# Kernel optimization log

Measured on AMD Instinct MI355X. Metric: run time of the kernel, lower is better.

Reference implementation:

```python
import jax, jax.numpy as jnp
import numpy as np
from jax import lax

NUM_SEGMENTS = 50
HIDDEN = 128
IN_CH = 64
LOGSIG_DIM = IN_CH + IN_CH * (IN_CH - 1) // 2 + IN_CH  # level1 + Levy area + startpoint


def setup_inputs() -> dict:
    key = jax.random.key(0)
    k0, k1, k2, k3, k4 = jax.random.split(key, 5)
    B, C, T, V = 16, IN_CH, 200, 25
    x = jax.random.normal(k0, (B, C, T, V), dtype=jnp.float32)
    s = 1.0 / np.sqrt(HIDDEN).astype(np.float32)
    W_ih = jax.random.uniform(k1, (4 * HIDDEN, LOGSIG_DIM), jnp.float32, -s, s)
    W_hh = jax.random.uniform(k2, (4 * HIDDEN, HIDDEN), jnp.float32, -s, s)
    b_ih = jax.random.uniform(k3, (4 * HIDDEN,), jnp.float32, -s, s)
    b_hh = jax.random.uniform(k4, (4 * HIDDEN,), jnp.float32, -s, s)
    return {"x": x, "W_ih": W_ih, "W_hh": W_hh, "b_ih": b_ih, "b_hh": b_hh}


def _segment_logsig(xn):
    # xn: (N, C, T). Split T into NUM_SEGMENTS chunks; level-2 log-signature per chunk.
    N, C, T = xn.shape
    L = T // NUM_SEGMENTS  # points per segment
    p = xn.transpose(0, 2, 1).reshape(N, NUM_SEGMENTS, L, C)  # path points
    start = p[:, :, 0]                                  # (N,S,C) segment startpoint
    inc = p[:, :, 1:] - p[:, :, :-1]                    # (N,S,L-1,C) increments
    dev = p[:, :, :-1] - start[:, :, None]              # (N,S,L-1,C) p_t - p_0
    # Level-2 iterated integrals (cross terms): S2_ij = sum_t dev_t,i * inc_t,j
    S2 = jnp.einsum('nsti,nstj->nsij', dev, inc)        # (N,S,C,C)
    A = 0.5 * (S2 - S2.transpose(0, 1, 3, 2))           # Levy area (antisymmetric part)
    iu, ju = jnp.triu_indices(C, k=1)
    levy = A[:, :, iu, ju]                              # (N,S,C(C-1)/2)
    lvl1 = p[:, :, -1] - start                          # (N,S,C) level-1 term
    return jnp.concatenate([lvl1, levy, start], axis=-1)  # (N,S,LOGSIG_DIM)


def _lstm(seq, W_ih, W_hh, b_ih, b_hh):
    # seq: (N, S, F). Single-layer unidirectional LSTM, torch gate order (i,f,g,o).
    N = seq.shape[0]
    x_proj = jnp.einsum('nsf,gf->nsg', seq, W_ih) + b_ih + b_hh  # (N,S,4H)

    def step(carry, xt):
        h, c = carry
        gates = xt + h @ W_hh.T
        i, f, g, o = jnp.split(gates, 4, axis=-1)
        c = jax.nn.sigmoid(f) * c + jax.nn.sigmoid(i) * jnp.tanh(g)
        h = jax.nn.sigmoid(o) * jnp.tanh(c)
        return (h, c), h

    h0 = jnp.zeros((N, HIDDEN), seq.dtype)
    c0 = jnp.zeros((N, HIDDEN), seq.dtype)
    _, hs = lax.scan(step, (h0, c0), x_proj.transpose(1, 0, 2))
    return hs.transpose(1, 0, 2)  # (N,S,H)


def reference(x, W_ih, W_hh, b_ih, b_hh):
    B, C, T, V = x.shape
    xn = x.transpose(0, 3, 1, 2).reshape(B * V, C, T)
    ls = _segment_logsig(xn)                      # (B*V, S, LOGSIG_DIM)
    h = _lstm(ls, W_ih, W_hh, b_ih, b_hh)          # (B*V, S, H)
    out = h.reshape(B, V, NUM_SEGMENTS, HIDDEN).transpose(0, 3, 2, 1)
    return out  # (B, H, S, V)
```

## Files before the change

kernel.cpp:

```cpp
#include <hip/hip_runtime.h>
#include <stdint.h>

#define NSEG 50
#define HID 128
#define KDIM 2144
#define KD2 2240
#define KD2B 4480
#define NROW 20000
#define NROW_PAD 20000
#define GATES 512
#define NSEQ 400
#define NGRP 528

typedef __attribute__((ext_vector_type(8))) _Float16 f16x8;
typedef __attribute__((ext_vector_type(4))) _Float16 f16x4;
typedef __attribute__((ext_vector_type(4))) float f32x4;
typedef __attribute__((ext_vector_type(4))) uint32_t u32x4;

#define GLB_SPACE __attribute__((address_space(1)))
#define LDS_SPACE __attribute__((address_space(3)))

__device__ __forceinline__ void g2lds16(const void* g, void* l) {
    __builtin_amdgcn_global_load_lds((const GLB_SPACE uint32_t*)g,
                                     (LDS_SPACE uint32_t*)l, 16, 0, 0);
}

__device__ __forceinline__ int goff528(int i) {
    int n = 63 - i;
    int q = n >> 2, t = n & 3;
    return NGRP - (q + 1) * (2 * q + t);
}
__device__ __forceinline__ int ifromg(int g) {
    int i = 63 - (int)sqrtf(8.0f * (float)(NGRP - g));
    if (i < 0) i = 0;
    if (i > 62) i = 62;
    while (i > 0 && goff528(i) > g) i--;
    while (goff528(i + 1) <= g) i++;
    return i;
}

#define UVP(c) ((((c) & 3) << 4) | ((c) >> 2))

__global__ __launch_bounds__(512) void feat_kernel(const float* __restrict__ x,
                                                   const float* __restrict__ Wih,
                                                   const float* __restrict__ Whh,
                                                   const float* __restrict__ bih,
                                                   const float* __restrict__ bhh,
                                                   _Float16* __restrict__ feat,
                                                   _Float16* __restrict__ wh,
                                                   _Float16* __restrict__ whh16,
                                                   float* __restrict__ bias) {
    int bid = blockIdx.x;
    int tid = threadIdx.x;

    __shared__ float pbuf[64 * 101];
    __shared__ __align__(16) float4 uv4[25 * 64];

    if (bid >= 800) {
        int* kmap = (int*)pbuf;
        for (int k = tid; k < KD2; k += 512) {
            int orig;
            if (k < 64) {
                orig = k;
            } else if (k < 64 + 4 * NGRP) {
                int g = (k - 64) >> 2, p = (k - 64) & 3;
                int i = ifromg(g);
                int j = i + 1 + 4 * (g - goff528(i)) + p;
                orig = (j < 64) ? (64 + 63 * i - (i * (i - 1)) / 2 + (j - i - 1)) : -1;
            } else {
                orig = 2080 + (k - (64 + 4 * NGRP));
            }
            kmap[k] = orig;
        }
        __syncthreads();
        const int nwih = 512 * KD2;
        const int nwhh = 512 * HID;
        const int total = nwih + nwhh + 512;
        for (int idx = (bid - 800) * 512 + tid; idx < total; idx += 64 * 512) {
            if (idx < nwih) {
                int row = idx / KD2;
                int k = idx - row * KD2;
                int orig = kmap[k];
                wh[idx] = (orig >= 0) ? (_Float16)Wih[row * KDIM + orig] : (_Float16)0.0f;
            } else if (idx < nwih + nwhh) {
                int q = idx - nwih;
                whh16[q] = (_Float16)Whh[q];
            } else {
                int g = idx - nwih - nwhh;
                bias[g] = bih[g] + bhh[g];
            }
        }
        return;
    }

    int b = bid / NSEG;
    int s = bid - b * NSEG;

    for (int i = tid; i < 6400; i += 512) {
        int c = i / 100;
        int r = i - c * 100;
        pbuf[c * 101 + r] = x[(((size_t)b * 64 + c) * 200 + 4 * s) * 25 + r];
    }
    __syncthreads();

    for (int i = tid; i < 1600; i += 512) {
        int v = i >> 6;
        int c = i & 63;
        float p0 = pbuf[c * 101 + v];
        float p1 = pbuf[c * 101 + 25 + v];
        float p2 = pbuf[c * 101 + 50 + v];
        float p3 = pbuf[c * 101 + 75 + v];
        uv4[v * 64 + UVP(c)] = make_float4(p1 - p0, p2 - p0, p2 - p1, p3 - p2);
        size_t m = ((size_t)(b * 25 + v)) * NSEG + s;
        feat[m * KD2 + c] = (_Float16)(p3 - p0);
        feat[m * KD2 + (64 + 4 * NGRP) + c] = (_Float16)p0;
    }
    __syncthreads();

    for (int idx = tid; idx < 4 * NGRP; idx += 512) {
        int vb = idx / NGRP;
        int g = idx - vb * NGRP;
        int i = ifromg(g);
        int t = g - goff528(i);
        int j0 = i + 1 + 4 * t;
        int k0 = 64 + 4 * g;
        float msk[4];
        int jc[4];
#pragma unroll
        for (int p = 0; p < 4; p++) {
            int j = j0 + p;
            msk[p] = (j < 64) ? 0.5f : 0.0f;
            jc[p] = (j < 64) ? UVP(j) : UVP(63);
        }
        int ip = UVP(i);
        int v0 = (vb == 0) ? 0 : 6 * vb + 1;
        int vn = (vb == 0) ? 7 : 6;
        for (int vv = 0; vv < vn; vv++) {
            int v = v0 + vv;
            const float4* rowv = &uv4[v * 64];
            float4 a = rowv[ip];
            f16x4 o;
#pragma unroll
            for (int p = 0; p < 4; p++) {
                float4 bb = rowv[jc[p]];
                float val = msk[p] * (a.x * bb.z - bb.x * a.z + a.y * bb.w - bb.y * a.w);
                o[p] = (_Float16)val;
            }
            size_t m = ((size_t)(b * 25 + v)) * NSEG + s;
            *(f16x4*)(feat + m * KD2 + k0) = o;
        }
    }
}

__global__ __launch_bounds__(64, 1) void gemm_kernel(const _Float16* __restrict__ feat,
                                                     const _Float16* __restrict__ wh,
                                                     const float* __restrict__ bias,
                                                     _Float16* __restrict__ xproj2) {
    int bid = blockIdx.x;
    int xcd = bid & 7;
    int idx = bid >> 3;
    int wg = xcd * 125 + idx;
    int mt = wg >> 2;
    int nb = wg & 3;
    int m0 = mt * 80;
    int n0 = nb * 128;
    int lane = threadIdx.x;
    int quad = lane >> 4;
    int l15 = lane & 15;

    __shared__ __align__(16) char lds[2][13312];

    const f32x4 z4 = {0.f, 0.f, 0.f, 0.f};
    f32x4 acc[5][8];
#pragma unroll
    for (int i = 0; i < 5; i++)
#pragma unroll
        for (int j = 0; j < 8; j++) acc[i][j] = z4;

    int lr = lane >> 2;
    int lc = (lane & 3) * 16;
    const char* aS[5];
    const char* bS[8];
#pragma unroll
    for (int u = 0; u < 5; u++)
        aS[u] = (const char*)feat + (size_t)(m0 + u * 16 + lr) * KD2B + lc;
#pragma unroll
    for (int u = 0; u < 8; u++)
        bS[u] = (const char*)wh + (size_t)(n0 + u * 16 + lr) * KD2B + lc;

#define STAGE(h_) do {                                                        \
        char* Hb = lds[(h_) & 1];                                             \
        size_t kb = (size_t)(h_) * 64;                                        \
        for (int u = 0; u < 5; u++) g2lds16(aS[u] + kb, Hb + u * 1024);       \
        for (int u = 0; u < 8; u++) g2lds16(bS[u] + kb, Hb + 5120 + u * 1024);\
    } while (0)

#define GPHASE(h_, VMLIT, DO_STAGE) do {                                      \
        asm volatile("s_waitcnt vmcnt(" #VMLIT ")" ::: "memory");             \
        const char* Hc = lds[(h_) & 1];                                       \
        f16x8 af[5], bf[8];                                                   \
        for (int tt = 0; tt < 5; tt++)                                        \
            af[tt] = *(const f16x8*)(Hc + (tt * 16 + l15) * 64 + quad * 16);  \
        for (int tt = 0; tt < 8; tt++)                                        \
            bf[tt] = *(const f16x8*)(Hc + 5120 + (tt * 16 + l15) * 64 + quad * 16); \
        asm volatile("s_waitcnt lgkmcnt(0)" ::: "memory");                    \
        __builtin_amdgcn_sched_barrier(0);                                    \
        if (DO_STAGE) STAGE((h_) + 2);                                        \
        for (int mtl = 0; mtl < 5; mtl++)                                     \
            for (int ntl = 0; ntl < 8; ntl++)                                 \
                acc[mtl][ntl] = __builtin_amdgcn_mfma_f32_16x16x32_f16(af[mtl], bf[ntl], acc[mtl][ntl], 0, 0, 0); \
    } while (0)

    STAGE(0);
    STAGE(1);

    for (int h = 0; h < 68; h++) GPHASE(h, 13, true);
    GPHASE(68, 13, false);
    GPHASE(69, 0, false);

#undef GPHASE
#undef STAGE

    float bv[8];
#pragma unroll
    for (int ntl = 0; ntl < 8; ntl++) bv[ntl] = bias[n0 + ntl * 16 + l15];

    _Float16* ep = (_Float16*)lds;
    for (int p = 0; p < 5; p++) {
#pragma unroll
        for (int ntl = 0; ntl < 8; ntl++)
#pragma unroll
            for (int r = 0; r < 4; r++)
                ep[(quad * 4 + r) * 132 + ntl * 16 + l15] =
                    (_Float16)(acc[p][ntl][r] + bv[ntl]);
        asm volatile("s_waitcnt lgkmcnt(0)" ::: "memory");
#pragma unroll
        for (int t = 0; t < 4; t++) {
            int rr = t * 4 + quad;
            int m = m0 + p * 16 + rr;
            unsigned q = (unsigned)m / 50u;
            unsigned s = (unsigned)m - q * 50u;
            const char* src = (const char*)ep + rr * 264 + l15 * 16;
            char* dst = (char*)xproj2 + ((size_t)s * NSEQ + q) * 1024 + (size_t)n0 * 2 + l15 * 16;
            *(u32x4*)dst = *(const u32x4*)src;
        }
        asm volatile("s_waitcnt lgkmcnt(0)" ::: "memory");
    }
}

__global__ __launch_bounds__(512, 2) void lstm_kernel(const _Float16* __restrict__ xproj2,
                                                      const _Float16* __restrict__ whh,
                                                      _Float16* __restrict__ hseq) {
    int bid = blockIdx.x;
    int tid = threadIdx.x;
    int wave = tid >> 6;
    int lane = tid & 63;
    int quad = lane >> 4;
    int col = lane & 15;
    int hid = wave * 16 + col;

    __shared__ __align__(16) char xbuf[25 * 4 * 1040];
    __shared__ __align__(16) _Float16 hst[NSEG * 4 * HID];
    __shared__ __align__(16) _Float16 hbuf[2][4 * 144];

    f16x8 bfrag[4][4];
    for (int g = 0; g < 4; g++) {
        int n = g * 128 + hid;
        for (int kq = 0; kq < 4; kq++)
            bfrag[g][kq] = *(const f16x8*)(whh + (size_t)n * HID + kq * 32 + quad * 8);
    }
    for (int i = tid; i < 2 * 4 * 144; i += 512) ((_Float16*)hbuf)[i] = (_Float16)0.0f;
    float cst = 0.0f;

    const char* xsrc = (const char*)xproj2;
    for (int r = wave; r < 100; r += 8)
        g2lds16(xsrc + ((size_t)((r >> 2) * NSEQ + bid * 4 + (r & 3))) * 1024 + lane * 16,
                xbuf + r * 1040);
    __syncthreads();

    const f32x4 z4 = {0.f, 0.f, 0.f, 0.f};
    for (int half = 0; half < 2; half++) {
        for (int ss = 0; ss < 25; ss++) {
            int s = half * 25 + ss;
            int cur = s & 1;
            int nxt = cur ^ 1;

            f16x8 afrag[4];
            for (int kq = 0; kq < 4; kq++)
                afrag[kq] = *(const f16x8*)(&hbuf[cur][(col & 3) * 144 + kq * 32 + quad * 8]);

            float xp[4];
            for (int g = 0; g < 4; g++)
                xp[g] = (float)(*(const _Float16*)(xbuf + (ss * 4 + quad) * 1040 +
                               (g * 128 + hid) * 2));

            f32x4 acc[4];
            for (int g = 0; g < 4; g++) {
                acc[g] = z4;
                for (int kq = 0; kq < 4; kq++)
                    acc[g] = __builtin_amdgcn_mfma_f32_16x16x32_f16(afrag[kq], bfrag[g][kq], acc[g], 0, 0, 0);
            }

            float gv[4];
            for (int g = 0; g < 4; g++) {
                float lo = (quad & 1) ? acc[g][1] : acc[g][0];
                float hi = (quad & 1) ? acc[g][3] : acc[g][2];
                gv[g] = (quad & 2) ? hi : lo;
            }

            float ip = gv[0] + xp[0];
            float fp = gv[1] + xp[1];
            float gp = gv[2] + xp[2];
            float op = gv[3] + xp[3];
            float si = __fdividef(1.0f, 1.0f + __expf(-ip));
            float sf = __fdividef(1.0f, 1.0f + __expf(-fp));
            float so = __fdividef(1.0f, 1.0f + __expf(-op));
            float eg = __expf(-2.0f * gp);
            float tg = __fdividef(1.0f - eg, 1.0f + eg);
            cst = sf * cst + si * tg;
            float ec = __expf(-2.0f * cst);
            float tc = __fdividef(1.0f - ec, 1.0f + ec);
            float hv = so * tc;
            _Float16 hv16 = (_Float16)hv;
            hbuf[nxt][quad * 144 + hid] = hv16;
            hst[(s * 4 + quad) * 128 + hid] = hv16;
            __syncthreads();
        }
        if (half == 0) {
            for (int r = wave; r < 100; r += 8)
                g2lds16(xsrc + ((size_t)((25 + (r >> 2)) * NSEQ + bid * 4 + (r & 3))) * 1024 + lane * 16,
                        xbuf + r * 1040);
            __syncthreads();
        }
    }

    const u32x4* src = (const u32x4*)hst;
    for (int i = tid; i < 3200; i += 512) {
        int s = i >> 6;
        int rem = i & 63;
        int seq = rem >> 4;
        int seg = rem & 15;
        u32x4 v = src[i];
        *(u32x4*)((char*)hseq + ((size_t)(s * NSEQ + bid * 4 + seq)) * 256 + seg * 16) = v;
    }
}

__global__ __launch_bounds__(256) void tr_kernel(const _Float16* __restrict__ hseq,
                                                 float* __restrict__ out) {
    int bid = blockIdx.x;
    int b = bid / NSEG;
    int s = bid - b * NSEG;
    int tid = threadIdx.x;

    __shared__ _Float16 buf[25 * 130];

    const uint32_t* src32 = (const uint32_t*)(hseq + ((size_t)s * NSEQ + b * 25) * HID);
    uint32_t* buf32 = (uint32_t*)buf;
    for (int i = tid; i < 1600; i += 256) {
        int v = i >> 6;
        int d = i & 63;
        buf32[v * 65 + d] = src32[i];
    }
    __syncthreads();
    for (int i = tid; i < 3200; i += 256) {
        int hid = i / 25;
        int v = i - hid * 25;
        out[(((size_t)b * 128 + hid) * NSEG + s) * 25 + v] = (float)buf[v * 130 + hid];
    }
}

extern "C" void kernel_launch(void* const* d_in, const int* in_sizes, int n_in,
                              void* d_out, int out_size, void* d_ws, size_t ws_size,
                              hipStream_t stream) {
    const float* x = (const float*)d_in[0];
    const float* Wih = (const float*)d_in[1];
    const float* Whh = (const float*)d_in[2];
    const float* bih = (const float*)d_in[3];
    const float* bhh = (const float*)d_in[4];
    float* out = (float*)d_out;

    char* ws = (char*)d_ws;
    size_t off = 0;
    _Float16* feat = (_Float16*)(ws + off);   off += (size_t)NROW_PAD * KD2 * 2;
    _Float16* xproj2 = (_Float16*)(ws + off); off += (size_t)NSEG * NSEQ * GATES * 2;
    _Float16* hseq = (_Float16*)(ws + off);   off += (size_t)NSEG * NSEQ * HID * 2;
    _Float16* wh = (_Float16*)(ws + off);     off += (size_t)512 * KD2 * 2;
    _Float16* whh16 = (_Float16*)(ws + off);  off += (size_t)512 * HID * 2;
    float* bias = (float*)(ws + off);         off += 512 * 4;

    hipLaunchKernelGGL(feat_kernel, dim3(864), dim3(512), 0, stream,
                       x, Wih, Whh, bih, bhh, feat, wh, whh16, bias);
    hipLaunchKernelGGL(gemm_kernel, dim3(1000), dim3(64), 0, stream, feat, wh, bias, xproj2);
    hipLaunchKernelGGL(lstm_kernel, dim3(100), dim3(512), 0, stream, xproj2, whh16, hseq);
    hipLaunchKernelGGL(tr_kernel, dim3(16 * NSEG), dim3(256), 0, stream, hseq, out);
}
```

Measured before the change: 213.1 us.

## Triple-buffer GEMM LDS staging and double-buffer MFMA operand registers

Moves the projection GEMM from a two-stage to a three-stage LDS ring, issuing the global-to-LDS copy into the buffer just consumed. The next step's fragments are read from LDS into a second register set while the current 40 MFMAs run. The staging lane-to-row mapping changes so each lane's LDS slot matches its fragment, making the reads one contiguous stride per lane. This aims to hide global and LDS latency behind matrix math, at the cost of more LDS and more fragment registers.

Measured after the change: 265.4 us. 1.25x slower.

```diff
diff --git a/kernel.cpp b/kernel.cpp
--- a/kernel.cpp
+++ b/kernel.cpp
@@ -168,7 +168,7 @@
     int quad = lane >> 4;
     int l15 = lane & 15;
 
-    __shared__ __align__(16) char lds[2][13312];
+    __shared__ __align__(16) char lds[3][13312];
 
     const f32x4 z4 = {0.f, 0.f, 0.f, 0.f};
     f32x4 acc[5][8];
@@ -177,48 +177,76 @@
 #pragma unroll
         for (int j = 0; j < 8; j++) acc[i][j] = z4;
 
-    int lr = lane >> 2;
-    int lc = (lane & 3) * 16;
+    int sr = lane & 15;
+    int sc = (lane >> 4) * 16;
     const char* aS[5];
     const char* bS[8];
 #pragma unroll
     for (int u = 0; u < 5; u++)
-        aS[u] = (const char*)feat + (size_t)(m0 + u * 16 + lr) * KD2B + lc;
+        aS[u] = (const char*)feat + (size_t)(m0 + u * 16 + sr) * KD2B + sc;
 #pragma unroll
     for (int u = 0; u < 8; u++)
-        bS[u] = (const char*)wh + (size_t)(n0 + u * 16 + lr) * KD2B + lc;
-
-#define STAGE(h_) do {                                                        \
-        char* Hb = lds[(h_) & 1];                                             \
-        size_t kb = (size_t)(h_) * 64;                                        \
-        for (int u = 0; u < 5; u++) g2lds16(aS[u] + kb, Hb + u * 1024);       \
-        for (int u = 0; u < 8; u++) g2lds16(bS[u] + kb, Hb + 5120 + u * 1024);\
+        bS[u] = (const char*)wh + (size_t)(n0 + u * 16 + sr) * KD2B + sc;
+
+#define STAGE(BUF, KB) do {                                                   \
+        for (int u = 0; u < 5; u++) g2lds16(aS[u] + (KB), (BUF) + u * 1024);  \
+        for (int u = 0; u < 8; u++) g2lds16(bS[u] + (KB), (BUF) + 5120 + u * 1024); \
     } while (0)
 
-#define GPHASE(h_, VMLIT, DO_STAGE) do {                                      \
-        asm volatile("s_waitcnt vmcnt(" #VMLIT ")" ::: "memory");             \
-        const char* Hc = lds[(h_) & 1];                                       \
-        f16x8 af[5], bf[8];                                                   \
-        for (int tt = 0; tt < 5; tt++)                                        \
-            af[tt] = *(const f16x8*)(Hc + (tt * 16 + l15) * 64 + quad * 16);  \
-        for (int tt = 0; tt < 8; tt++)                                        \
-            bf[tt] = *(const f16x8*)(Hc + 5120 + (tt * 16 + l15) * 64 + quad * 16); \
+#define READF(BUF, FA, FB) do {                                               \
+        const char* rb_ = (BUF) + lane * 16;                                  \
+        for (int tt = 0; tt < 5; tt++) FA[tt] = *(const f16x8*)(rb_ + tt * 1024); \
+        for (int tt = 0; tt < 8; tt++) FB[tt] = *(const f16x8*)(rb_ + 5120 + tt * 1024); \
+    } while (0)
+
+#define MFMA40(FA, FB) do {                                                   \
+        for (int mtl = 0; mtl < 5; mtl++)                                     \
+            for (int ntl = 0; ntl < 8; ntl++)                                 \
+                acc[mtl][ntl] = __builtin_amdgcn_mfma_f32_16x16x32_f16(FA[mtl], FB[ntl], acc[mtl][ntl], 0, 0, 0); \
+    } while (0)
+
+#define GPHASE(BC, BN, FCA, FCB, FNA, FNB, KB3, VMLIT, DO_STAGE, DO_READN) do { \
         asm volatile("s_waitcnt lgkmcnt(0)" ::: "memory");                    \
         __builtin_amdgcn_sched_barrier(0);                                    \
-        if (DO_STAGE) STAGE((h_) + 2);                                        \
-        for (int mtl = 0; mtl < 5; mtl++)                                     \
-            for (int ntl = 0; ntl < 8; ntl++)                                 \
-                acc[mtl][ntl] = __builtin_amdgcn_mfma_f32_16x16x32_f16(af[mtl], bf[ntl], acc[mtl][ntl], 0, 0, 0); \
+        if (DO_STAGE) STAGE(BC, KB3);                                         \
+        asm volatile("s_waitcnt vmcnt(" #VMLIT ")" ::: "memory");             \
+        __builtin_amdgcn_sched_barrier(0);                                    \
+        if (DO_READN) READF(BN, FNA, FNB);                                    \
+        __builtin_amdgcn_sched_barrier(0);                                    \
+        MFMA40(FCA, FCB);                                                     \
     } while (0)
 
-    STAGE(0);
-    STAGE(1);
-
-    for (int h = 0; h < 68; h++) GPHASE(h, 13, true);
-    GPHASE(68, 13, false);
-    GPHASE(69, 0, false);
+    char* B0 = lds[0];
+    char* B1 = lds[1];
+    char* B2 = lds[2];
+
+    f16x8 fAa[5], fAb[8], fBa[5], fBb[8];
+
+    STAGE(B0, 0);
+    STAGE(B1, 64);
+    STAGE(B2, 128);
+    asm volatile("s_waitcnt vmcnt(26)" ::: "memory");
+    __builtin_amdgcn_sched_barrier(0);
+    READF(B0, fAa, fAb);
+
+    size_t kb3 = 192;
+    for (int it = 0; it < 33; it++) {
+        GPHASE(B0, B1, fAa, fAb, fBa, fBb, kb3, 26, 1, 1);
+        kb3 += 64;
+        GPHASE(B1, B2, fBa, fBb, fAa, fAb, kb3, 26, 1, 1);
+        kb3 += 64;
+        char* t = B0; B0 = B2; B2 = B1; B1 = t;
+    }
+    GPHASE(B0, B1, fAa, fAb, fBa, fBb, kb3, 26, 1, 1);
+    GPHASE(B1, B2, fBa, fBb, fAa, fAb, 0, 13, 0, 1);
+    GPHASE(B2, B0, fAa, fAb, fBa, fBb, 0, 0, 0, 1);
+    asm volatile("s_waitcnt lgkmcnt(0)" ::: "memory");
+    __builtin_amdgcn_sched_barrier(0);
+    MFMA40(fBa, fBb);
 
 #undef GPHASE
+#undef MFMA40
+#undef READF
 #undef STAGE
 
     float bv[8];
```
